# Kernel optimization log

Hardware: AMD Instinct MI355X
Metric: run time of the kernel (lower is better)

## Reference

```python
import jax, jax.numpy as jnp
import numpy as np

B, N, H, F, DIN, NC = 4, 1024, 8, 256, 256, 10  # batch graphs, nodes, heads, feat/head, input dim, classes


def setup_inputs() -> dict:
    key = jax.random.key(0)
    ks = jax.random.split(key, 12)
    def rn(k, shape, s=0.05):
        return jax.random.normal(k, shape, jnp.float32) * s
    return dict(
        features=rn(ks[0], (B, N, DIN), 1.0),
        eigvects=rn(ks[1], (B, N, DIN), 1.0),  # unused by forward, mirrors original signature
        attn_mask=jnp.zeros((B, N, N), jnp.float32),  # additive mask: 0 = edge, -inf = no edge
        W1=rn(ks[2], (DIN, H * F)), a_src1=rn(ks[3], (H, F)), a_tgt1=rn(ks[4], (H, F)),
        skip1=rn(ks[5], (DIN, H * F)), b1=jnp.zeros((H * F,), jnp.float32),
        W2=rn(ks[6], (H * F, H * F)), a_src2=rn(ks[7], (H, F)), a_tgt2=rn(ks[8], (H, F)),
        skip2=rn(ks[9], (H * F, H * F)), b2=jnp.zeros((F,), jnp.float32),
        Wc=rn(ks[10], (F, NC)), bc=jnp.zeros((NC,), jnp.float32),
    )


def _gat_layer(x, mask, W, a_s, a_t, skipW, b, concat):
    # GAT IMP2: dense all-pairs scores + additive connectivity mask. Dropout is eval-mode identity.
    Bb, Nn, _ = x.shape
    Hh, Ff = a_s.shape
    p = (x @ W).reshape(Bb, Nn, Hh, Ff)                      # projected node features (B,N,H,F)
    s_src = jnp.einsum('bnhf,hf->bnh', p, a_s)
    s_tgt = jnp.einsum('bnhf,hf->bnh', p, a_t)
    # score[b,i,j,h] = leaky(src_i + tgt_j) + mask[b,i,j]
    scores = jax.nn.leaky_relu(s_src[:, :, None, :] + s_tgt[:, None, :, :], 0.2) + mask[..., None]
    attn = jax.nn.softmax(scores, axis=2)                    # softmax over neighbors j
    out = jnp.einsum('bijh,bjhf->bihf', attn, p)
    out = out + (x @ skipW).reshape(Bb, Nn, Hh, Ff)          # skip connection (projected)
    out = out.reshape(Bb, Nn, Hh * Ff) if concat else out.mean(axis=2)
    out = out + b
    return jax.nn.elu(out) if concat else out


def reference(features, eigvects, attn_mask, W1, a_src1, a_tgt1, skip1, b1,
              W2, a_src2, a_tgt2, skip2, b2, Wc, bc):
    x = _gat_layer(features, attn_mask, W1, a_src1, a_tgt1, skip1, b1, True)   # (B,N,H*F), ELU
    x = _gat_layer(x, attn_mask, W2, a_src2, a_tgt2, skip2, b2, False)         # (B,N,F), heads averaged
    g = x.mean(axis=1)                                                         # mean pool over nodes
    return g @ Wc + bc                                                         # (B, n_classes)
```

## Files before the change

kernel.cpp:

```cpp
#include <hip/hip_runtime.h>
#include <hip/hip_bf16.h>
#include <stdint.h>
#include <stddef.h>

typedef __hip_bfloat16 bf16;
typedef __attribute__((ext_vector_type(8))) short bhalf8;
typedef __attribute__((ext_vector_type(4))) short short4v;
typedef __attribute__((ext_vector_type(4))) float floatx4;

static __device__ __forceinline__ float b2f(bf16 v) { return __bfloat162float(v); }
static __device__ __forceinline__ bf16  f2b(float v) { return __float2bfloat16(v); }
static __device__ __forceinline__ short f2s(float v) {
    union { bf16 b; short s; } u; u.b = __float2bfloat16(v); return u.s;
}
static __device__ __forceinline__ float s2f(short v) {
    union { short s; bf16 b; } u; u.s = v; return b2f(u.b);
}

static __device__ __forceinline__ float loadf(const void* p, size_t i, int f32) {
    return f32 ? ((const float*)p)[i] : b2f(((const bf16*)p)[i]);
}

static __device__ __forceinline__ void gl_lds16(const void* g, void* l) {
    __builtin_amdgcn_global_load_lds(
        (const __attribute__((address_space(1))) void*)g,
        (__attribute__((address_space(3))) void*)l, 16, 0, 0);
}

static __device__ __forceinline__ void load_mask4b(const bf16* m, size_t idx,
                                                   float* mv) {
    short4v v = *(const short4v*)(m + idx);
    #pragma unroll
    for (int t = 0; t < 4; t++) mv[t] = s2f(v[t]);
}

__global__ __launch_bounds__(256) void prep_k(const void* __restrict__ feat,
                                              bf16* __restrict__ featc,
                                              const void* __restrict__ mask,
                                              bf16* __restrict__ maskb,
                                              float* __restrict__ zbase, int nzero,
                                              const void* __restrict__ W1,
                                              bf16* __restrict__ W1t,
                                              const void* __restrict__ skip1,
                                              bf16* __restrict__ S1t,
                                              const void* __restrict__ W2,
                                              const void* __restrict__ a_src1,
                                              const void* __restrict__ a_tgt1,
                                              const void* __restrict__ a_src2,
                                              const void* __restrict__ a_tgt2,
                                              bf16* __restrict__ Wa1b,
                                              bf16* __restrict__ Wa2b,
                                              int* __restrict__ flagp)
{
    __shared__ int sflag;
    __shared__ bf16 tile[32][33];
    const int tid = threadIdx.x;

    if (tid < 64) {
        const unsigned short* s = (const unsigned short*)W1;
        int bad = 0;
        #pragma unroll
        for (int i = 0; i < 4; i++) {
            int e = (s[tid * 4 + i] >> 7) & 0xFF;
            if (e > 0x85 || (e != 0 && e < 0x60)) bad++;
        }
        bad += __shfl_xor(bad, 1, 64);
        bad += __shfl_xor(bad, 2, 64);
        bad += __shfl_xor(bad, 4, 64);
        bad += __shfl_xor(bad, 8, 64);
        bad += __shfl_xor(bad, 16, 64);
        bad += __shfl_xor(bad, 32, 64);
        if (tid == 0) sflag = (bad > 16) ? 1 : 0;
    }
    __syncthreads();
    const int f32 = sflag;

    int id = blockIdx.x;
    if (id == 0 && tid == 0) *flagp = f32;

    if (id < 4096) {
        const int i = id * 256 + tid;
        featc[i] = f32 ? f2b(((const float*)feat)[i]) : ((const bf16*)feat)[i];
        return;
    }
    id -= 4096;
    if (id < 4096) {
        const size_t i = (size_t)id * 1024 + tid * 4;
        if (f32) {
            float4 v = *(const float4*)((const float*)mask + i);
            short4v o;
            o[0] = f2s(v.x); o[1] = f2s(v.y); o[2] = f2s(v.z); o[3] = f2s(v.w);
            *(short4v*)(maskb + i) = o;
        } else {
            *(short4v*)(maskb + i) = *(const short4v*)((const bf16*)mask + i);
        }
        return;
    }
    id -= 4096;
    if (id < 480) {
        const int i = id * 256 + tid;
        if (i < nzero) zbase[i] = 0.f;
        return;
    }
    id -= 480;
    if (id < 1024) {
        const void* in = (id < 512) ? W1 : skip1;
        bf16* out = (id < 512) ? W1t : S1t;
        const int t = id & 511;
        const int bx = t & 63, byy = t >> 6;
        const int tx = tid & 31, ty = tid >> 5;
        const int c0 = bx * 32, r0 = byy * 32;
        #pragma unroll
        for (int yy = ty; yy < 32; yy += 8)
            tile[yy][tx] = f2b(loadf(in, (size_t)(r0 + yy) * 2048 + c0 + tx, f32));
        __syncthreads();
        #pragma unroll
        for (int yy = ty; yy < 32; yy += 8)
            out[(size_t)(c0 + yy) * 256 + r0 + tx] = tile[tx][yy];
        return;
    }
    id -= 1024;
    if (id < 512) {
        const int wave = tid >> 6, lane = tid & 63;
        const int base = id * 64;
        const int hh = base >> 11, h = hh & 7;
        const void* a = (hh < 8) ? a_src2 : a_tgt2;
        float av[4];
        #pragma unroll
        for (int i = 0; i < 4; i++) av[i] = loadf(a, h * 256 + lane * 4 + i, f32);
        #pragma unroll 4
        for (int o = 0; o < 16; o++) {
            const int idx = base + wave * 16 + o;
            const int k = idx & 2047;
            float acc = 0.f;
            #pragma unroll
            for (int i = 0; i < 4; i++)
                acc = fmaf(loadf(W2, (size_t)k * 2048 + h * 256 + lane * 4 + i, f32),
                           av[i], acc);
            #pragma unroll
            for (int off2 = 32; off2; off2 >>= 1) acc += __shfl_down(acc, off2, 64);
            if (lane == 0) Wa2b[idx] = f2b(acc);
        }
        return;
    }
    id -= 512;
    {
        const int wave = tid >> 6, lane = tid & 63;
        const int base = id * 64;
        const int hh = base >> 8, h = hh & 7;
        const void* a = (hh < 8) ? a_src1 : a_tgt1;
        float av[4];
        #pragma unroll
        for (int i = 0; i < 4; i++) av[i] = loadf(a, h * 256 + lane * 4 + i, f32);
        #pragma unroll 4
        for (int o = 0; o < 16; o++) {
            const int idx = base + wave * 16 + o;
            const int k = idx & 255;
            float acc = 0.f;
            #pragma unroll
            for (int i = 0; i < 4; i++)
                acc = fmaf(loadf(W1, (size_t)k * 2048 + h * 256 + lane * 4 + i, f32),
                           av[i], acc);
            #pragma unroll
            for (int off2 = 32; off2; off2 >>= 1) acc += __shfl_down(acc, off2, 64);
            if (lane == 0) Wa1b[idx] = f2b(acc);
        }
    }
}

__global__ __launch_bounds__(256) void gemm_dual(const bf16* __restrict__ featc,
                                                 const bf16* __restrict__ W1t,
                                                 const bf16* __restrict__ S1t,
                                                 bf16* __restrict__ pT,
                                                 bf16* __restrict__ sk1)
{
    __shared__ __align__(16) short sA[128][32];
    __shared__ __align__(16) short sB[128][32];
    const int tid = threadIdx.x;
    const int z = blockIdx.z;
    const bf16* A  = z ? featc : W1t;
    const bf16* Bt = z ? S1t   : featc;
    const int mbase = (z ? blockIdx.x : blockIdx.y) * 128;
    const int nbase = (z ? blockIdx.y : blockIdx.x) * 128;
    const int wave = tid >> 6, lane = tid & 63;
    const int wm = wave >> 1, wn = wave & 1;
    const int lrow = lane & 15, quad = lane >> 4;

    floatx4 acc[4][4];
    #pragma unroll
    for (int i = 0; i < 4; i++)
        #pragma unroll
        for (int j = 0; j < 4; j++)
            acc[i][j] = (floatx4){0.f, 0.f, 0.f, 0.f};

    const int srow = wave * 32 + (lane >> 2);
    const int scol = (lane & 3) * 8;
    const bf16* gA0 = A  + (size_t)(mbase + srow) * 256 + scol;
    const bf16* gA1 = gA0 + (size_t)16 * 256;
    const bf16* gB0 = Bt + (size_t)(nbase + srow) * 256 + scol;
    const bf16* gB1 = gB0 + (size_t)16 * 256;
    char* lA0 = (char*)&sA[0][0] + wave * 2048 + lane * 16;
    char* lA1 = lA0 + 1024;
    char* lB0 = (char*)&sB[0][0] + wave * 2048 + lane * 16;
    char* lB1 = lB0 + 1024;

    for (int k0 = 0; k0 < 256; k0 += 32) {
        __syncthreads();
        gl_lds16(gA0 + k0, lA0);
        gl_lds16(gA1 + k0, lA1);
        gl_lds16(gB0 + k0, lB0);
        gl_lds16(gB1 + k0, lB1);
        __syncthreads();
        bhalf8 af[4], bfr[4];
        #pragma unroll
        for (int t = 0; t < 4; t++) af[t]  = *(const bhalf8*)&sA[wm * 64 + t * 16 + lrow][quad * 8];
        #pragma unroll
        for (int t = 0; t < 4; t++) bfr[t] = *(const bhalf8*)&sB[wn * 64 + t * 16 + lrow][quad * 8];
        #pragma unroll
        for (int tm = 0; tm < 4; tm++)
            #pragma unroll
            for (int tn = 0; tn < 4; tn++)
                acc[tm][tn] = __builtin_amdgcn_mfma_f32_16x16x32_bf16(af[tm], bfr[tn], acc[tm][tn], 0, 0, 0);
    }

    #pragma unroll
    for (int tm = 0; tm < 4; tm++) {
        #pragma unroll
        for (int tn = 0; tn < 4; tn++) {
            const int col = nbase + wn * 64 + tn * 16 + lrow;
            #pragma unroll
            for (int r = 0; r < 4; r++) {
                const int row = mbase + wm * 64 + tm * 16 + quad * 4 + r;
                if (z) {
                    sk1[(size_t)row * 2048 + col] = f2b(acc[tm][tn][r]);
                } else {
                    const size_t idx = ((size_t)((col >> 10) * 8 + (row >> 8)) << 18)
                                     + (size_t)(row & 255) * 1024 + (col & 1023);
                    pT[idx] = f2b(acc[tm][tn][r]);
                }
            }
        }
    }
}

template <int K>
__global__ __launch_bounds__(256) void score_k(const bf16* __restrict__ X,
                                               const bf16* __restrict__ Wab,
                                               float* __restrict__ ss,
                                               float* __restrict__ st)
{
    constexpr int VPL = K / 64;
    const int wave = threadIdx.x >> 6, lane = threadIdx.x & 63;
    const int n = blockIdx.x * 4 + wave;
    const int b = n >> 10, nn = n & 1023;

    const bf16* xr = X + (size_t)n * K + lane * VPL;
    float xv[VPL];
    if (VPL == 4) {
        short4v v = *(const short4v*)xr;
        #pragma unroll
        for (int t = 0; t < 4; t++) xv[t] = s2f(v[t]);
    } else {
        #pragma unroll
        for (int c = 0; c < VPL / 8; c++) {
            bhalf8 v = *(const bhalf8*)(xr + c * 8);
            #pragma unroll
            for (int t = 0; t < 8; t++) xv[c * 8 + t] = s2f(v[t]);
        }
    }

    #pragma unroll
    for (int hh = 0; hh < 16; hh++) {
        const bf16* wr = Wab + (size_t)hh * K + lane * VPL;
        float acc = 0.f;
        if (VPL == 4) {
            short4v v = *(const short4v*)wr;
            #pragma unroll
            for (int t = 0; t < 4; t++) acc = fmaf(xv[t], s2f(v[t]), acc);
        } else {
            #pragma unroll
            for (int c = 0; c < VPL / 8; c++) {
                bhalf8 v = *(const bhalf8*)(wr + c * 8);
                #pragma unroll
                for (int t = 0; t < 8; t++) acc = fmaf(xv[c * 8 + t], s2f(v[t]), acc);
            }
        }
        #pragma unroll
        for (int off = 32; off; off >>= 1) acc += __shfl_down(acc, off, 64);
        if (lane == 0) {
            const int h = hh & 7;
            if (hh < 8) ss[(b * 8 + h) * 1024 + nn] = acc;
            else        st[(b * 8 + h) * 1024 + nn] = acc;
        }
    }
}

__global__ __launch_bounds__(256) void attn_fused(const float* __restrict__ s_src_t,
                                                  const float* __restrict__ s_tgt_t,
                                                  const bf16* __restrict__ maskb,
                                                  const bf16* __restrict__ pT,
                                                  const bf16* __restrict__ sk,
                                                  const void* __restrict__ bias,
                                                  bf16* __restrict__ x2,
                                                  const int* __restrict__ flag)
{
    __shared__ __align__(16) short sA[2][64][32];
    __shared__ __align__(16) short sB[2][128][32];
    __shared__ short sStgt[1024];
    __shared__ float sInvl[64];

    const int tid = threadIdx.x;
    const int d = blockIdx.x;
    const int by = d & 15, fh = (d >> 4) & 1, bh = d >> 5;
    const int b = bh >> 3, h = bh & 7;
    const int f32 = *flag;
    const int wave = tid >> 6, lane = tid & 63;
    const int lrow = lane & 15, quad = lane >> 4;

    #pragma unroll
    for (int q = 0; q < 4; q++)
        sStgt[q * 256 + tid] = f2s(s_tgt_t[bh * 1024 + q * 256 + tid]);

    const int row  = tid >> 2;
    const int col0 = (tid & 3) * 8;
    const float ssr = s_src_t[bh * 1024 + by * 64 + row];
    const size_t mrow0 = ((size_t)(b * 1024 + by * 64 + row)) << 10;

    const bf16* gB = pT + ((size_t)bh << 18)
                   + (size_t)(fh * 128 + wave * 32 + (lane >> 2)) * 1024
                   + (lane & 3) * 8;

    floatx4 acc[4][2];
    #pragma unroll
    for (int i = 0; i < 4; i++)
        #pragma unroll
        for (int j = 0; j < 2; j++)
            acc[i][j] = (floatx4){0.f, 0.f, 0.f, 0.f};

    float lacc = 0.f;

    auto stageB = [&](int k0, int buf) {
        char* l = (char*)&sB[buf][0][0] + wave * 2048 + lane * 16;
        #pragma unroll
        for (int c = 0; c < 2; c++)
            gl_lds16(gB + (size_t)(c * 16) * 1024 + k0, l + c * 1024);
    };
    auto genA = [&](int k0, int buf, bhalf8 m8) {
        const short* sp = &sStgt[k0 + col0];
        bhalf8 ev;
        #pragma unroll
        for (int t = 0; t < 8; t++) {
            float x = ssr + s2f(sp[t]);
            x = fmaxf(x, 0.2f * x);
            float e = __expf(x + s2f(m8[t]));
            lacc += e;
            ev[t] = f2s(e);
        }
        *(bhalf8*)&sA[buf][row][col0] = ev;
    };
    auto loadmask = [&](int k0) -> bhalf8 {
        return *(const bhalf8*)(maskb + mrow0 + k0 + col0);
    };
    auto mfma_step = [&](int cur) {
        bhalf8 af[4], bfr[2];
        #pragma unroll
        for (int mt = 0; mt < 4; mt++)
            af[mt] = *(const bhalf8*)&sA[cur][mt * 16 + lrow][quad * 8];
        #pragma unroll
        for (int nt = 0; nt < 2; nt++)
            bfr[nt] = *(const bhalf8*)&sB[cur][wave * 32 + nt * 16 + lrow][quad * 8];
        #pragma unroll
        for (int mt = 0; mt < 4; mt++)
            #pragma unroll
            for (int nt = 0; nt < 2; nt++)
                acc[mt][nt] = __builtin_amdgcn_mfma_f32_16x16x32_bf16(af[mt], bfr[nt], acc[mt][nt], 0, 0, 0);
    };

    bhalf8 mcur = loadmask(0);
    stageB(0, 0);
    asm volatile("s_waitcnt lgkmcnt(0)\n\ts_barrier" ::: "memory");
    genA(0, 0, mcur);
    bhalf8 mnxt = loadmask(32);

    int cur = 0;
    for (int k0 = 0; k0 < 992; k0 += 32, cur ^= 1) {
        asm volatile("s_waitcnt lgkmcnt(0)\n\ts_barrier" ::: "memory");
        stageB(k0 + 32, cur ^ 1);
        genA(k0 + 32, cur ^ 1, mnxt);
        if (k0 + 64 < 1024)
            mnxt = loadmask(k0 + 64);
        asm volatile("s_waitcnt vmcnt(3)" ::: "memory");
        __builtin_amdgcn_sched_barrier(0);
        mfma_step(cur);
    }
    asm volatile("s_waitcnt lgkmcnt(0)\n\ts_barrier" ::: "memory");
    asm volatile("s_waitcnt vmcnt(0)" ::: "memory");
    __builtin_amdgcn_sched_barrier(0);
    mfma_step(cur);

    lacc += __shfl_xor(lacc, 1, 64);
    lacc += __shfl_xor(lacc, 2, 64);
    if ((tid & 3) == 0) sInvl[row] = 1.0f / lacc;
    __syncthreads();

    #pragma unroll
    for (int mt = 0; mt < 4; mt++) {
        #pragma unroll
        for (int r = 0; r < 4; r++) {
            const int rl = mt * 16 + quad * 4 + r;
            const int rg = by * 64 + rl;
            const float il = sInvl[rl];
            #pragma unroll
            for (int nt = 0; nt < 2; nt++) {
                const int col = fh * 128 + wave * 32 + nt * 16 + lrow;
                const int hf = h * 256 + col;
                const size_t idx = ((size_t)(b * 1024 + rg)) * 2048 + hf;
                float v = acc[mt][nt][r] * il + b2f(sk[idx]) + loadf(bias, hf, f32);
                v = (v > 0.f) ? v : expm1f(v);
                x2[idx] = f2b(v);
            }
        }
    }
}

__global__ __launch_bounds__(256) void colsoft_k(const float* __restrict__ s_src_t,
                                                 const float* __restrict__ s_tgt_t,
                                                 const bf16* __restrict__ maskb,
                                                 float* __restrict__ c)
{
    __shared__ float sS[64];
    __shared__ float sIl[64];
    const int bh = blockIdx.x, iz = blockIdx.y, b = bh >> 3;
    const int tid = threadIdx.x;
    const int i0 = iz * 64;
    if (tid < 64) sS[tid] = s_src_t[bh * 1024 + i0 + tid];
    __syncthreads();

    {
        const int row = tid >> 2, c4 = tid & 3;
        const float ssr = sS[row];
        const size_t mrow = ((size_t)(b * 1024 + i0 + row)) << 10;
        float l = 0.f;
        #pragma unroll 4
        for (int q = 0; q < 64; q++) {
            const int j = c4 * 256 + q * 4;
            float mv[4];
            load_mask4b(maskb, mrow + j, mv);
            float4 s4 = *(const float4*)(s_tgt_t + bh * 1024 + j);
            float sv[4] = {s4.x, s4.y, s4.z, s4.w};
            #pragma unroll
            for (int t = 0; t < 4; t++) {
                float x = ssr + sv[t];
                x = fmaxf(x, 0.2f * x);
                l += __expf(x + mv[t]);
            }
        }
        l += __shfl_xor(l, 1, 64);
        l += __shfl_xor(l, 2, 64);
        if ((tid & 3) == 0) sIl[row] = 1.0f / l;
    }
    __syncthreads();

    const int j0 = tid * 4;
    float4 s4 = *(const float4*)(s_tgt_t + bh * 1024 + j0);
    float sv[4] = {s4.x, s4.y, s4.z, s4.w};
    float a[4] = {0.f, 0.f, 0.f, 0.f};
    #pragma unroll 4
    for (int r = 0; r < 64; r++) {
        const float sr = sS[r], il = sIl[r];
        float mv[4];
        load_mask4b(maskb, (((size_t)(b * 1024 + i0 + r)) << 10) + j0, mv);
        #pragma unroll
        for (int t = 0; t < 4; t++) {
            float x = sr + sv[t];
            x = fmaxf(x, 0.2f * x);
            a[t] = fmaf(il, __expf(x + mv[t]), a[t]);
        }
    }
    #pragma unroll
    for (int t = 0; t < 4; t++)
        atomicAdd(&c[bh * 1024 + j0 + t], a[t]);
}

__global__ __launch_bounds__(256) void yx_k(const bf16* __restrict__ x2,
                                            const float* __restrict__ c,
                                            float* __restrict__ y,
                                            float* __restrict__ xbar)
{
    __shared__ float sC[8][32];
    const int b = blockIdx.x, kt = blockIdx.y, jc = blockIdx.z;
    const int t = threadIdx.x;
    const int k = kt * 512 + t * 2;
    const int j0 = jc * 32;
    {
        const int h = t >> 5, jj = t & 31;
        sC[h][jj] = c[(b * 8 + h) * 1024 + j0 + jj];
    }
    __syncthreads();
    float acc0[8] = {0.f, 0.f, 0.f, 0.f, 0.f, 0.f, 0.f, 0.f};
    float acc1[8] = {0.f, 0.f, 0.f, 0.f, 0.f, 0.f, 0.f, 0.f};
    float ax0 = 0.f, ax1 = 0.f;
    #pragma unroll 4
    for (int jj = 0; jj < 32; jj++) {
        const unsigned int v =
            *(const unsigned int*)&x2[((size_t)(b * 1024 + j0 + jj)) * 2048 + k];
        const float x0 = s2f((short)(v & 0xffff));
        const float x1 = s2f((short)(v >> 16));
        ax0 += x0; ax1 += x1;
        #pragma unroll
        for (int h = 0; h < 8; h++) {
            acc0[h] = fmaf(sC[h][jj], x0, acc0[h]);
            acc1[h] = fmaf(sC[h][jj], x1, acc1[h]);
        }
    }
    #pragma unroll
    for (int h = 0; h < 8; h++) {
        atomicAdd(&y[(b * 8 + h) * 2048 + k], acc0[h]);
        atomicAdd(&y[(b * 8 + h) * 2048 + k + 1], acc1[h]);
    }
    atomicAdd(&xbar[b * 2048 + k], ax0);
    atomicAdd(&xbar[b * 2048 + k + 1], ax1);
}

__global__ __launch_bounds__(256) void gs_k(const void* __restrict__ W2,
                                            const void* __restrict__ skip2,
                                            const float* __restrict__ y,
                                            const float* __restrict__ xbar,
                                            float* __restrict__ gA,
                                            float* __restrict__ gS,
                                            const int* __restrict__ flagp)
{
    __shared__ float sY[64];
    const int f32 = *flagp;
    int id = blockIdx.x;
    if (id < 1024) {
        const int bh = id & 31, kc = id >> 5;
        const int h = bh & 7, f = threadIdx.x;
        const int k0 = kc * 64;
        if (threadIdx.x < 64) sY[threadIdx.x] = y[bh * 2048 + k0 + threadIdx.x];
        __syncthreads();
        float acc = 0.f;
        #pragma unroll 4
        for (int kk = 0; kk < 64; kk++)
            acc = fmaf(sY[kk], loadf(W2, (size_t)(k0 + kk) * 2048 + h * 256 + f, f32), acc);
        atomicAdd(&gA[bh * 256 + f], acc);
    } else {
        const int idx = id - 1024;
        const int b = idx & 3, hft = (idx >> 2) & 7, kc = idx >> 5;
        const int hf = hft * 256 + threadIdx.x;
        const int k0 = kc * 64;
        if (threadIdx.x < 64) sY[threadIdx.x] = xbar[b * 2048 + k0 + threadIdx.x];
        __syncthreads();
        float acc = 0.f;
        #pragma unroll 4
        for (int kk = 0; kk < 64; kk++)
            acc = fmaf(sY[kk], loadf(skip2, (size_t)(k0 + kk) * 2048 + hf, f32), acc);
        atomicAdd(&gS[b * 2048 + hf], acc);
    }
}

__global__ __launch_bounds__(256) void classify2_k(const float* __restrict__ gA,
                                                   const float* __restrict__ gS,
                                                   const void* __restrict__ b2,
                                                   const void* __restrict__ Wc,
                                                   const void* __restrict__ bc,
                                                   void* __restrict__ out,
                                                   const int* __restrict__ flag)
{
    __shared__ float gv[256];
    const int f32 = *flag;
    const int b = blockIdx.x, f = threadIdx.x;
    float s = 0.f;
    #pragma unroll
    for (int h = 0; h < 8; h++)
        s += gA[(b * 8 + h) * 256 + f] + gS[b * 2048 + h * 256 + f];
    gv[f] = s * (1.0f / 8192.0f) + loadf(b2, f, f32);
    __syncthreads();
    if (f < 10) {
        float acc = loadf(bc, f, f32);
        for (int k = 0; k < 256; k++)
            acc = fmaf(gv[k], loadf(Wc, k * 10 + f, f32), acc);
        if (f32) ((float*)out)[b * 10 + f] = acc;
        else     ((bf16*)out)[b * 10 + f] = f2b(acc);
    }
}

extern "C" void kernel_launch(void* const* d_in, const int* in_sizes, int n_in,
                              void* d_out, int out_size, void* d_ws, size_t ws_size,
                              hipStream_t stream)
{
    (void)in_sizes; (void)n_in; (void)out_size; (void)ws_size;
    const void* feat   = d_in[0];
    const void* mask   = d_in[2];
    const void* W1     = d_in[3];
    const void* a_src1 = d_in[4];
    const void* a_tgt1 = d_in[5];
    const void* skip1  = d_in[6];
    const void* b1     = d_in[7];
    const void* W2     = d_in[8];
    const void* a_src2 = d_in[9];
    const void* a_tgt2 = d_in[10];
    const void* skip2  = d_in[11];
    const void* b2v    = d_in[12];
    const void* Wc     = d_in[13];
    const void* bc     = d_in[14];

    char* ws = (char*)d_ws;
    size_t off = 0;
    auto alloc = [&](size_t bytes) -> void* {
        void* p = ws + off;
        off += (bytes + 255) & ~(size_t)255;
        return p;
    };
    int*   flag  = (int*)alloc(256);
    bf16*  featc = (bf16*)alloc(4096ull * 256 * 2);
    bf16*  maskb = (bf16*)alloc(4ull * 1024 * 1024 * 2);
    bf16*  W1t   = (bf16*)alloc(2048ull * 256 * 2);
    bf16*  S1t   = (bf16*)alloc(2048ull * 256 * 2);
    bf16*  sk1   = (bf16*)alloc(4096ull * 2048 * 2);
    bf16*  x2    = (bf16*)alloc(4096ull * 2048 * 2);
    bf16*  pT    = (bf16*)alloc(4096ull * 2048 * 2);
    float* ss    = (float*)alloc(32ull * 1024 * 4);
    float* st    = (float*)alloc(32ull * 1024 * 4);
    bf16*  Wa1b  = (bf16*)alloc(16ull * 256 * 2);
    bf16*  Wa2b  = (bf16*)alloc(16ull * 2048 * 2);
    float* cbuf = (float*)alloc(32ull * 1024 * 4);
    float* gA   = (float*)alloc(32ull * 256 * 4);
    float* gS   = (float*)alloc(4ull * 2048 * 4);
    float* xbar = (float*)alloc(4ull * 2048 * 4);
    float* y    = (float*)alloc(32ull * 2048 * 4);
    const int nzero = 32768 + 3 * 8192 + 65536;

    prep_k<<<10272, 256, 0, stream>>>(feat, featc, mask, maskb, cbuf, nzero,
                                      W1, W1t, skip1, S1t, W2,
                                      a_src1, a_tgt1, a_src2, a_tgt2,
                                      Wa1b, Wa2b, flag);
    gemm_dual<<<dim3(32, 16, 2), 256, 0, stream>>>(featc, W1t, S1t, pT, sk1);
    score_k<256><<<1024, 256, 0, stream>>>(featc, Wa1b, ss, st);
    attn_fused<<<1024, 256, 0, stream>>>(ss, st, maskb, pT, sk1, b1, x2, flag);
    score_k<2048><<<1024, 256, 0, stream>>>(x2, Wa2b, ss, st);
    colsoft_k<<<dim3(32, 16), 256, 0, stream>>>(ss, st, maskb, cbuf);
    yx_k<<<dim3(4, 4, 32), 256, 0, stream>>>(x2, cbuf, y, xbar);
    gs_k<<<2048, 256, 0, stream>>>(W2, skip2, y, xbar, gA, gS, flag);
    classify2_k<<<4, 256, 0, stream>>>(gA, gS, b2v, Wc, bc, d_out, flag);
}
```

Before: 354.0 us.

## Compress additive attention mask to a bitmask shared by attention kernels

Prep now turns the additive mask into a 1-bit-per-edge bitmask (bit set where the value exceeds -1e30) in place of a bf16 copy. The attention and column-softmax kernels read those bits and zero the exponent for masked edges instead of adding the mask value. This cuts mask traffic by 16x against the bf16 copy. It assumes the mask holds only 0 or -inf; any finite non-zero mask values would no longer be applied.

```diff
diff --git a/kernel.cpp b/kernel.cpp
--- a/kernel.cpp
+++ b/kernel.cpp
@@ -27,17 +27,10 @@
         (__attribute__((address_space(3))) void*)l, 16, 0, 0);
 }
 
-static __device__ __forceinline__ void load_mask4b(const bf16* m, size_t idx,
-                                                   float* mv) {
-    short4v v = *(const short4v*)(m + idx);
-    #pragma unroll
-    for (int t = 0; t < 4; t++) mv[t] = s2f(v[t]);
-}
-
 __global__ __launch_bounds__(256) void prep_k(const void* __restrict__ feat,
                                               bf16* __restrict__ featc,
                                               const void* __restrict__ mask,
-                                              bf16* __restrict__ maskb,
+                                              unsigned int* __restrict__ maskbits,
                                               float* __restrict__ zbase, int nzero,
                                               const void* __restrict__ W1,
                                               bf16* __restrict__ W1t,
@@ -54,6 +47,7 @@
 {
     __shared__ int sflag;
     __shared__ bf16 tile[32][33];
+    __shared__ unsigned int nibs[256];
     const int tid = threadIdx.x;
 
     if (tid < 64) {
@@ -86,13 +80,26 @@
     id -= 4096;
     if (id < 4096) {
         const size_t i = (size_t)id * 1024 + tid * 4;
+        float mv[4];
         if (f32) {
             float4 v = *(const float4*)((const float*)mask + i);
-            short4v o;
-            o[0] = f2s(v.x); o[1] = f2s(v.y); o[2] = f2s(v.z); o[3] = f2s(v.w);
-            *(short4v*)(maskb + i) = o;
+            mv[0] = v.x; mv[1] = v.y; mv[2] = v.z; mv[3] = v.w;
         } else {
-            *(short4v*)(maskb + i) = *(const short4v*)((const bf16*)mask + i);
+            short4v v = *(const short4v*)((const bf16*)mask + i);
+            #pragma unroll
+            for (int t = 0; t < 4; t++) mv[t] = s2f(v[t]);
+        }
+        unsigned int n4 = 0;
+        #pragma unroll
+        for (int t = 0; t < 4; t++)
+            if (mv[t] > -1e30f) n4 |= (1u << t);
+        nibs[tid] = n4;
+        __syncthreads();
+        if (tid < 32) {
+            unsigned int w = 0;
+            #pragma unroll
+            for (int s = 0; s < 8; s++) w |= nibs[tid * 8 + s] << (s * 4);
+            maskbits[(size_t)id * 32 + tid] = w;
         }
         return;
     }
@@ -297,7 +304,7 @@
 
 __global__ __launch_bounds__(256) void attn_fused(const float* __restrict__ s_src_t,
                                                   const float* __restrict__ s_tgt_t,
-                                                  const bf16* __restrict__ maskb,
+                                                  const unsigned int* __restrict__ maskbits,
                                                   const bf16* __restrict__ pT,
                                                   const bf16* __restrict__ sk,
                                                   const void* __restrict__ bias,
@@ -324,7 +331,8 @@
     const int row  = tid >> 2;
     const int col0 = (tid & 3) * 8;
     const float ssr = s_src_t[bh * 1024 + by * 64 + row];
-    const size_t mrow0 = ((size_t)(b * 1024 + by * 64 + row)) << 10;
+    const unsigned int* gbitsrow = maskbits
+                                 + (size_t)(b * 1024 + by * 64 + row) * 32;
 
     const bf16* gB = pT + ((size_t)bh << 18)
                    + (size_t)(fh * 128 + wave * 32 + (lane >> 2)) * 1024
@@ -345,21 +353,22 @@
         for (int c = 0; c < 2; c++)
             gl_lds16(gB + (size_t)(c * 16) * 1024 + k0, l + c * 1024);
     };
-    auto genA = [&](int k0, int buf, bhalf8 m8) {
+    auto genA = [&](int k0, int buf, unsigned int bits8) {
         const short* sp = &sStgt[k0 + col0];
         bhalf8 ev;
         #pragma unroll
         for (int t = 0; t < 8; t++) {
             float x = ssr + s2f(sp[t]);
             x = fmaxf(x, 0.2f * x);
-            float e = __expf(x + s2f(m8[t]));
+            float e = __expf(x);
+            e = ((bits8 >> t) & 1u) ? e : 0.f;
             lacc += e;
             ev[t] = f2s(e);
         }
         *(bhalf8*)&sA[buf][row][col0] = ev;
     };
-    auto loadmask = [&](int k0) -> bhalf8 {
-        return *(const bhalf8*)(maskb + mrow0 + k0 + col0);
+    auto loadbits = [&](int k0) -> unsigned int {
+        return (gbitsrow[k0 >> 5] >> col0) & 0xFFu;
     };
     auto mfma_step = [&](int cur) {
         bhalf8 af[4], bfr[2];
@@ -376,11 +385,11 @@
                 acc[mt][nt] = __builtin_amdgcn_mfma_f32_16x16x32_bf16(af[mt], bfr[nt], acc[mt][nt], 0, 0, 0);
     };
 
-    bhalf8 mcur = loadmask(0);
+    unsigned int mcur = loadbits(0);
     stageB(0, 0);
     asm volatile("s_waitcnt lgkmcnt(0)\n\ts_barrier" ::: "memory");
     genA(0, 0, mcur);
-    bhalf8 mnxt = loadmask(32);
+    unsigned int mnxt = loadbits(32);
 
     int cur = 0;
     for (int k0 = 0; k0 < 992; k0 += 32, cur ^= 1) {
@@ -388,7 +397,7 @@
         stageB(k0 + 32, cur ^ 1);
         genA(k0 + 32, cur ^ 1, mnxt);
         if (k0 + 64 < 1024)
-            mnxt = loadmask(k0 + 64);
+            mnxt = loadbits(k0 + 64);
         asm volatile("s_waitcnt vmcnt(3)" ::: "memory");
         __builtin_amdgcn_sched_barrier(0);
         mfma_step(cur);
@@ -425,34 +434,39 @@
 
 __global__ __launch_bounds__(256) void colsoft_k(const float* __restrict__ s_src_t,
                                                  const float* __restrict__ s_tgt_t,
-                                                 const bf16* __restrict__ maskb,
+                                                 const unsigned int* __restrict__ maskbits,
                                                  float* __restrict__ c)
 {
     __shared__ float sS[64];
     __shared__ float sIl[64];
+    __shared__ unsigned int smb[64 * 32];
     const int bh = blockIdx.x, iz = blockIdx.y, b = bh >> 3;
     const int tid = threadIdx.x;
     const int i0 = iz * 64;
     if (tid < 64) sS[tid] = s_src_t[bh * 1024 + i0 + tid];
+    {
+        const unsigned int* gbits = maskbits + (size_t)(b * 1024 + i0) * 32;
+        #pragma unroll
+        for (int q = 0; q < 8; q++) smb[q * 256 + tid] = gbits[q * 256 + tid];
+    }
     __syncthreads();
 
     {
         const int row = tid >> 2, c4 = tid & 3;
         const float ssr = sS[row];
-        const size_t mrow = ((size_t)(b * 1024 + i0 + row)) << 10;
         float l = 0.f;
         #pragma unroll 4
         for (int q = 0; q < 64; q++) {
             const int j = c4 * 256 + q * 4;
-            float mv[4];
-            load_mask4b(maskb, mrow + j, mv);
+            const unsigned int nib = (smb[row * 32 + (j >> 5)] >> (j & 31)) & 15u;
             float4 s4 = *(const float4*)(s_tgt_t + bh * 1024 + j);
             float sv[4] = {s4.x, s4.y, s4.z, s4.w};
             #pragma unroll
             for (int t = 0; t < 4; t++) {
                 float x = ssr + sv[t];
                 x = fmaxf(x, 0.2f * x);
-                l += __expf(x + mv[t]);
+                float e = __expf(x);
+                l += ((nib >> t) & 1u) ? e : 0.f;
             }
         }
         l += __shfl_xor(l, 1, 64);
@@ -462,19 +476,20 @@
     __syncthreads();
 
     const int j0 = tid * 4;
+    const int wj = j0 >> 5, sh = j0 & 31;
     float4 s4 = *(const float4*)(s_tgt_t + bh * 1024 + j0);
     float sv[4] = {s4.x, s4.y, s4.z, s4.w};
     float a[4] = {0.f, 0.f, 0.f, 0.f};
     #pragma unroll 4
     for (int r = 0; r < 64; r++) {
         const float sr = sS[r], il = sIl[r];
-        float mv[4];
-        load_mask4b(maskb, (((size_t)(b * 1024 + i0 + r)) << 10) + j0, mv);
+        const unsigned int nib = (smb[r * 32 + wj] >> sh) & 15u;
         #pragma unroll
         for (int t = 0; t < 4; t++) {
             float x = sr + sv[t];
             x = fmaxf(x, 0.2f * x);
-            a[t] = fmaf(il, __expf(x + mv[t]), a[t]);
+            float e = ((nib >> t) & 1u) ? __expf(x) : 0.f;
+            a[t] = fmaf(il, e, a[t]);
         }
     }
     #pragma unroll
@@ -614,7 +629,7 @@
     };
     int*   flag  = (int*)alloc(256);
     bf16*  featc = (bf16*)alloc(4096ull * 256 * 2);
-    bf16*  maskb = (bf16*)alloc(4ull * 1024 * 1024 * 2);
+    unsigned int* maskbits = (unsigned int*)alloc(4096ull * 32 * 4);
     bf16*  W1t   = (bf16*)alloc(2048ull * 256 * 2);
     bf16*  S1t   = (bf16*)alloc(2048ull * 256 * 2);
     bf16*  sk1   = (bf16*)alloc(4096ull * 2048 * 2);
@@ -631,15 +646,15 @@
     float* y    = (float*)alloc(32ull * 2048 * 4);
     const int nzero = 32768 + 3 * 8192 + 65536;
 
-    prep_k<<<10272, 256, 0, stream>>>(feat, featc, mask, maskb, cbuf, nzero,
+    prep_k<<<10272, 256, 0, stream>>>(feat, featc, mask, maskbits, cbuf, nzero,
                                       W1, W1t, skip1, S1t, W2,
                                       a_src1, a_tgt1, a_src2, a_tgt2,
                                       Wa1b, Wa2b, flag);
     gemm_dual<<<dim3(32, 16, 2), 256, 0, stream>>>(featc, W1t, S1t, pT, sk1);
     score_k<256><<<1024, 256, 0, stream>>>(featc, Wa1b, ss, st);
-    attn_fused<<<1024, 256, 0, stream>>>(ss, st, maskb, pT, sk1, b1, x2, flag);
+    attn_fused<<<1024, 256, 0, stream>>>(ss, st, maskbits, pT, sk1, b1, x2, flag);
     score_k<2048><<<1024, 256, 0, stream>>>(x2, Wa2b, ss, st);
-    colsoft_k<<<dim3(32, 16), 256, 0, stream>>>(ss, st, maskb, cbuf);
+    colsoft_k<<<dim3(32, 16), 256, 0, stream>>>(ss, st, maskbits, cbuf);
     yx_k<<<dim3(4, 4, 32), 256, 0, stream>>>(x2, cbuf, y, xbar);
     gs_k<<<2048, 256, 0, stream>>>(W2, skip2, y, xbar, gA, gS, flag);
     classify2_k<<<4, 256, 0, stream>>>(gA, gS, b2v, Wc, bc, d_out, flag);
```

New measurement: 331.3 us. -6.4%, faster.
